# Kernel tuning notes

Measured on AMD Instinct MI355X. Metric: run time of the kernel, lower is better.

The kernel has to match this reference:

```python
import jax, jax.numpy as jnp
import numpy as np

B, K, G, C = 64, 4000, 200, 91
LAMBDA_BOX, LAMBDA_CLS, LAMBDA_OBJ = 5.0, 1.0, 1.0
EPS = 1e-9


def _make_boxes(key, lead_shape):
    k1, k2 = jax.random.split(key)
    tl = jax.random.uniform(k1, lead_shape + (2,)) * 0.7
    wh = jax.random.uniform(k2, lead_shape + (2,)) * 0.29 + 0.01
    return jnp.concatenate([tl, tl + wh], axis=-1)


def setup_inputs() -> dict:
    key = jax.random.key(0)
    ks = jax.random.split(key, 6)
    pred_boxes = _make_boxes(ks[0], (B, K))
    pred_obj_logits = jax.random.normal(ks[1], (B, K), dtype=jnp.float32)
    pred_cls_logits = jax.random.normal(ks[2], (B, K, C), dtype=jnp.float32)
    gt_boxes = _make_boxes(ks[3], (B, G))
    gt_labels = jax.random.randint(ks[4], (B, G), 0, C)
    n_gt = jax.random.randint(ks[5], (B,), 1, G + 1)
    gt_mask = jnp.arange(G)[None, :] < n_gt[:, None]
    return dict(pred_boxes=pred_boxes, pred_obj_logits=pred_obj_logits,
                pred_cls_logits=pred_cls_logits, gt_boxes=gt_boxes,
                gt_labels=gt_labels, gt_mask=gt_mask)


def _area(x):
    return jnp.clip(x[..., 2] - x[..., 0], 0.0) * jnp.clip(x[..., 3] - x[..., 1], 0.0)


def _pairwise_iou(a, b):
    # a: (K,4), b: (G,4) -> (K,G)
    tl = jnp.maximum(a[:, None, :2], b[None, :, :2])
    br = jnp.minimum(a[:, None, 2:], b[None, :, 2:])
    wh = jnp.clip(br - tl, 0.0)
    inter = wh[..., 0] * wh[..., 1]
    union = jnp.clip(_area(a)[:, None] + _area(b)[None, :] - inter, EPS)
    return inter / union


def _ciou_loss(pb, gb):
    # pb, gb: (M,4) matched pairs; elementwise CIoU loss = 1 - CIoU
    tl = jnp.maximum(pb[:, :2], gb[:, :2])
    br = jnp.minimum(pb[:, 2:], gb[:, 2:])
    wh = jnp.clip(br - tl, 0.0)
    inter = wh[:, 0] * wh[:, 1]
    iou = inter / jnp.clip(_area(pb) + _area(gb) - inter, EPS)
    px = (pb[:, 0] + pb[:, 2]) * 0.5
    py = (pb[:, 1] + pb[:, 3]) * 0.5
    tx = (gb[:, 0] + gb[:, 2]) * 0.5
    ty = (gb[:, 1] + gb[:, 3]) * 0.5
    rho2 = (px - tx) ** 2 + (py - ty) ** 2
    etl = jnp.minimum(pb[:, :2], gb[:, :2])
    ebr = jnp.maximum(pb[:, 2:], gb[:, 2:])
    c2 = jnp.clip((ebr[:, 0] - etl[:, 0]) ** 2 + (ebr[:, 1] - etl[:, 1]) ** 2, EPS)
    pw = jnp.clip(pb[:, 2] - pb[:, 0], EPS)
    ph = jnp.clip(pb[:, 3] - pb[:, 1], EPS)
    tw = jnp.clip(gb[:, 2] - gb[:, 0], EPS)
    th = jnp.clip(gb[:, 3] - gb[:, 1], EPS)
    v = (4.0 / jnp.pi ** 2) * (jnp.arctan(tw / th) - jnp.arctan(pw / ph)) ** 2
    alpha = jax.lax.stop_gradient(v / (1.0 - iou + v + EPS))  # torch.no_grad
    return 1.0 - (iou - rho2 / c2 - alpha * v)


def _greedy_match(iou0):
    # iou0: (K,G), invalid gt columns pre-masked to -1. Fixed min(K,G)-step
    # argmax-and-mask scan reproducing the torch greedy loop (break -> valid=False).
    Gd = iou0.shape[1]
    steps = min(iou0.shape[0], Gd)

    def step(m, _):
        flat = jnp.argmax(m)
        p = flat // Gd
        g = flat % Gd
        valid = m.reshape(-1)[flat] >= 0.0
        m2 = m.at[p, :].set(-1.0).at[:, g].set(-1.0)
        return jnp.where(valid, m2, m), (p, g, valid)

    _, (ps, gs, vs) = jax.lax.scan(step, iou0, None, length=steps)
    return ps, gs, vs


def _per_batch(pred_b, cls_b, gt_b, labels_b, mask_b):
    iou = jax.lax.stop_gradient(_pairwise_iou(pred_b, gt_b))  # matching is non-diff (.item() in torch)
    iou = jnp.where(mask_b[None, :], iou, -1.0)
    ps, gs, vs = _greedy_match(iou)
    vf = vs.astype(pred_b.dtype)
    n = jnp.sum(vf)
    denom = jnp.maximum(n, 1.0)
    pb = pred_b[ps]
    gb = gt_b[gs]
    lbox = jnp.sum(_ciou_loss(pb, gb) * vf) / denom
    logp = jax.nn.log_softmax(cls_b[ps], axis=-1)
    lce = -jnp.take_along_axis(logp, labels_b[gs][:, None], axis=1)[:, 0]
    lcls = jnp.sum(lce * vf) / denom
    obj_tgt = jnp.zeros((pred_b.shape[0],), pred_b.dtype).at[
        jnp.where(vs, ps, pred_b.shape[0])].set(1.0, mode='drop')
    return lbox, lcls, obj_tgt, n > 0.0


def reference(pred_boxes, pred_obj_logits, pred_cls_logits, gt_boxes, gt_labels, gt_mask):
    lbox_b, lcls_b, obj_tgt, has = jax.vmap(_per_batch)(
        pred_boxes, pred_cls_logits, gt_boxes, gt_labels, gt_mask)
    hf = has.astype(pred_boxes.dtype)
    nb = jnp.maximum(jnp.sum(hf), 1.0)
    loss_box = jnp.sum(lbox_b * hf) / nb
    loss_cls = jnp.sum(lcls_b * hf) / nb
    # BCEWithLogits(mean): softplus(x) - t*x
    loss_obj = jnp.mean(jax.nn.softplus(pred_obj_logits) - obj_tgt * pred_obj_logits)
    total = LAMBDA_BOX * loss_box + LAMBDA_CLS * loss_cls + LAMBDA_OBJ * loss_obj
    return total, loss_box, loss_cls, loss_obj
```

## Files before the change

### kernel.cpp

```cpp
#include <hip/hip_runtime.h>
#include <math.h>

#define B_ 64
#define K_ 4000
#define G_ 200
#define C_ 91
#define EPS_ 1e-9f
#define NW_ 16
#define DEPTH_ 32
typedef unsigned long long ull;

#define WS_FLAG 0
#define WS_PART 256
#define WS_TOP 327680

__device__ __forceinline__ float box_area(float4 a) {
#pragma clang fp contract(off)
  return fmaxf(a.z - a.x, 0.f) * fmaxf(a.w - a.y, 0.f);
}

__device__ __forceinline__ float iou_ab(float4 a, float aA, float4 b, float aB) {
#pragma clang fp contract(off)
  float tlx = fmaxf(a.x, b.x), tly = fmaxf(a.y, b.y);
  float brx = fminf(a.z, b.z), bry = fminf(a.w, b.w);
  float w = fmaxf(brx - tlx, 0.f), h = fmaxf(bry - tly, 0.f);
  float inter = w * h;
  float uni = fmaxf(aA + aB - inter, EPS_);
  return inter / uni;
}

__device__ __forceinline__ float ciou_loss(float4 p, float4 g) {
  float tlx = fmaxf(p.x, g.x), tly = fmaxf(p.y, g.y);
  float brx = fminf(p.z, g.z), bry = fminf(p.w, g.w);
  float w = fmaxf(brx - tlx, 0.f), h = fmaxf(bry - tly, 0.f);
  float inter = w * h;
  float areaP = fmaxf(p.z - p.x, 0.f) * fmaxf(p.w - p.y, 0.f);
  float areaG = fmaxf(g.z - g.x, 0.f) * fmaxf(g.w - g.y, 0.f);
  float iou = inter / fmaxf(areaP + areaG - inter, EPS_);
  float px = (p.x + p.z) * 0.5f, py = (p.y + p.w) * 0.5f;
  float tx = (g.x + g.z) * 0.5f, ty = (g.y + g.w) * 0.5f;
  float rho2 = (px - tx) * (px - tx) + (py - ty) * (py - ty);
  float ex = fmaxf(p.z, g.z) - fminf(p.x, g.x);
  float ey = fmaxf(p.w, g.w) - fminf(p.y, g.y);
  float c2 = fmaxf(ex * ex + ey * ey, EPS_);
  float pw = fmaxf(p.z - p.x, EPS_), ph = fmaxf(p.w - p.y, EPS_);
  float tw = fmaxf(g.z - g.x, EPS_), th = fmaxf(g.w - g.y, EPS_);
  float dat = atanf(tw / th) - atanf(pw / ph);
  float v = (4.0f / (float)(M_PI * M_PI)) * dat * dat;
  float alpha = v / ((1.f - iou) + v + EPS_);
  return 1.f - (iou - rho2 / c2 - alpha * v);
}

__global__ void kdetect(const unsigned char* m8, int* flag) {
  int b = threadIdx.x;
  int ok = 1;
  const unsigned char* r = m8 + b * G_;
  if (r[0] != 1) ok = 0;
  int seen0 = 0;
  for (int g = 0; g < G_; ++g) {
    unsigned char c = r[g];
    if (c > 1) { ok = 0; break; }
    if (c == 0) seen0 = 1;
    else if (seen0) { ok = 0; break; }
  }
  int all = __all(ok);
  if (b == 0) *flag = all ? 1 : 0;
}

__device__ __forceinline__ float block_sum(float v, float* s_red) {
  for (int off = 32; off > 0; off >>= 1) v += __shfl_xor(v, off);
  int lane = threadIdx.x & 63, wid = threadIdx.x >> 6;
  if (lane == 0) s_red[wid] = v;
  __syncthreads();
  float r = 0.f;
  if (wid == 0) {
    float t = (lane < NW_) ? s_red[lane] : 0.f;
    for (int off = 32; off > 0; off >>= 1) t += __shfl_xor(t, off);
    r = t;
  }
  __syncthreads();
  return r;
}

__device__ __forceinline__ ull wave_maxkey(ull k) {
  for (int off = 32; off > 0; off >>= 1) {
    ull o = __shfl_xor(k, off);
    if (o > k) k = o;
  }
  return k;
}

#define TOP4_INS(key)                                   \
  if ((key) > t3) {                                     \
    t3 = (key);                                         \
    ull tmp_;                                           \
    if (t3 > t2) { tmp_ = t2; t2 = t3; t3 = tmp_; }     \
    if (t2 > t1) { tmp_ = t1; t1 = t2; t2 = tmp_; }     \
    if (t1 > t0) { tmp_ = t0; t0 = t1; t1 = tmp_; }     \
  }

#define TOP8_INS(key)                                   \
  if ((key) > t7) {                                     \
    t7 = (key);                                         \
    ull tmp_;                                           \
    if (t7 > t6) { tmp_ = t6; t6 = t7; t7 = tmp_; }     \
    if (t6 > t5) { tmp_ = t5; t5 = t6; t6 = tmp_; }     \
    if (t5 > t4) { tmp_ = t4; t4 = t5; t5 = tmp_; }     \
    if (t4 > t3) { tmp_ = t3; t3 = t4; t4 = tmp_; }     \
    if (t3 > t2) { tmp_ = t2; t2 = t3; t3 = tmp_; }     \
    if (t2 > t1) { tmp_ = t1; t1 = t2; t2 = tmp_; }     \
    if (t1 > t0) { tmp_ = t0; t0 = t1; t1 = tmp_; }     \
  }

__global__ __launch_bounds__(1024) void kinit(const float* __restrict__ pred_boxes,
                                              const float* __restrict__ gt_boxes,
                                              const void* __restrict__ gt_mask,
                                              char* __restrict__ ws) {
  __shared__ float4 s_p[K_];
  const int blk = blockIdx.x;
  const int b = blk >> 3, oct = blk & 7;
  const int tid = threadIdx.x, lane = tid & 63, wid = tid >> 6;
  const int msk8 = *(const int*)(ws + WS_FLAG);
  const float4* p4 = (const float4*)pred_boxes + (size_t)b * K_;
  const float4* g4 = (const float4*)gt_boxes + (size_t)b * G_;

  for (int i = tid; i < K_; i += 1024) s_p[i] = p4[i];
  __syncthreads();

  ull* wtop = (ull*)(ws + WS_TOP);
  for (int cc = wid; cc < 25; cc += 16) {
    const int col = oct * 25 + cc;
    ull* dst = wtop + ((size_t)b * G_ + col) * DEPTH_;
    int v;
    if (msk8) v = ((const unsigned char*)gt_mask)[(size_t)b * G_ + col] != 0;
    else      v = ((const int*)gt_mask)[(size_t)b * G_ + col] != 0;
    if (!v) {
      for (int o = lane; o < DEPTH_; o += 64) dst[o] = 0ull;
      continue;
    }
    float4 gb = g4[col];
    float gA = box_area(gb);
    ull t0 = 0, t1 = 0, t2 = 0, t3 = 0;
#pragma unroll 2
    for (int k = lane; k < K_; k += 64) {
      float4 pb = s_p[k];
      float iou = iou_ab(pb, box_area(pb), gb, gA);
      ull e = ((ull)__float_as_uint(iou) << 12) | (ull)(4095 - k);
      TOP4_INS(e);
    }
    int supplied = 0, written = 0;
    for (int o = 0; o < DEPTH_; ++o) {
      ull m = wave_maxkey(t0);
      if (m == 0ull) break;
      int dn = 0;
      if (t0 == m) {
        t0 = t1; t1 = t2; t2 = t3; t3 = 0;
        if (++supplied == 4) dn = 1;
      }
      if (lane == 0) dst[o] = m;
      ++written;
      if (__any(dn)) break;
    }
    for (int o = written + lane; o < DEPTH_; o += 64) dst[o] = 0ull;
  }
}

__global__ __launch_bounds__(1024) void kmerged(
    const float* __restrict__ pred_boxes, const float* __restrict__ obj_logits,
    const float* __restrict__ cls_logits, const float* __restrict__ gt_boxes,
    const int* __restrict__ gt_labels, char* __restrict__ ws) {
  __shared__ float s_gx[G_], s_gy[G_], s_gz[G_], s_gw[G_], s_garea[G_];
  __shared__ unsigned char s_rowused[4096];
  __shared__ ull s_toplist[G_][DEPTH_ + 1];
  __shared__ int s_mp[G_];
  __shared__ unsigned short s_mg[G_];
  __shared__ int s_cnt;
  __shared__ float s_red[NW_];
  const int b = blockIdx.x;
  const int tid = threadIdx.x, lane = tid & 63, wid = tid >> 6;
  const float4* p4 = (const float4*)pred_boxes + (size_t)b * K_;
  const float4* g4 = (const float4*)gt_boxes + (size_t)b * G_;
  const ull* wtop = (const ull*)(ws + WS_TOP);

  for (int g = tid; g < G_; g += 1024) {
    float4 gb = g4[g];
    s_gx[g] = gb.x; s_gy[g] = gb.y; s_gz[g] = gb.z; s_gw[g] = gb.w;
    s_garea[g] = box_area(gb);
  }
  for (int k = tid; k < 4096; k += 1024) s_rowused[k] = 0;
  for (int i = tid; i < G_ * DEPTH_; i += 1024)
    s_toplist[i / DEPTH_][i % DEPTH_] = wtop[((size_t)b * G_) * DEPTH_ + i];
  __syncthreads();

  if (wid == 0) {
    ull key0 = 0, key1 = 0, key2 = 0, key3 = 0;
    int ptr0 = DEPTH_, ptr1 = DEPTH_, ptr2 = DEPTH_, ptr3 = DEPTH_;
    int cloc = 0;
#define SLOTINIT(S)                                                        \
    { int col = S * 64 + lane;                                             \
      if (col < G_) {                                                      \
        ull h_ = s_toplist[col][0];                                        \
        if (h_ != 0ull) {                                                  \
          key##S = (h_ << 8) | (ull)(255 - col); ptr##S = 1; ++cloc; } } }
    SLOTINIT(0) SLOTINIT(1) SLOTINIT(2) SLOTINIT(3)
#undef SLOTINIT
    for (int off = 32; off > 0; off >>= 1) cloc += __shfl_xor(cloc, off);
    const int cnt = cloc;
    if (lane == 0) s_cnt = cnt;

    for (int step = 0; step < cnt;) {
      ull a1 = key0, a2 = key1;
      if (key1 > key0) { a1 = key1; a2 = key0; }
      if (key2 > a1) { a2 = a1; a1 = key2; } else if (key2 > a2) a2 = key2;
      if (key3 > a1) { a2 = a1; a1 = key3; } else if (key3 > a2) a2 = key3;
      for (int off = 32; off > 0; off >>= 1) {
        ull b1 = __shfl_xor(a1, off), b2 = __shfl_xor(a2, off);
        if (b1 > a1) { a2 = (a1 > b2) ? a1 : b2; a1 = b1; }
        else { a2 = (b1 > a2) ? b1 : a2; }
      }
      const int p1 = 4095 - (int)((a1 >> 8) & 0xFFF);
      const int g1v = 255 - (int)(a1 & 0xFF);
      const int p2 = 4095 - (int)((a2 >> 8) & 0xFFF);
      const int g2v = 255 - (int)(a2 & 0xFF);
      const bool do2 = (a2 != 0ull) && (p2 != p1) && (step + 1 < cnt);
      if (lane == 0) {
        s_mp[step] = p1; s_mg[step] = (unsigned short)g1v; s_rowused[p1] = 1;
        if (do2) { s_mp[step + 1] = p2; s_mg[step + 1] = (unsigned short)g2v; s_rowused[p2] = 1; }
      }
      __builtin_amdgcn_wave_barrier();
      const int gd2 = do2 ? g2v : -1;
      const int pd2 = do2 ? p2 : -1;
      int need = 0;
#define DEMOTE(S)                                                           \
      { int col = S * 64 + lane; ull kk = key##S;                           \
        if (kk != 0ull) {                                                   \
          if (col == g1v || col == gd2) { key##S = 0ull; }                  \
          else { int krow = 4095 - (int)((kk >> 8) & 0xFFF);                \
            if (krow == p1 || krow == pd2) {                                \
              ull nk = 0ull; int np = ptr##S;                               \
              while (np < DEPTH_) {                                         \
                ull e = s_toplist[col][np]; ++np;                           \
                if (e == 0ull) { np = DEPTH_; break; }                      \
                int pr = 4095 - (int)((e >> 12) & 0xFFF);                   \
                if (!s_rowused[pr]) { nk = (e << 8) | (ull)(255 - col); break; } \
              }                                                             \
              ptr##S = np; key##S = nk;                                     \
              if (nk == 0ull) need |= (1 << S); } } } }
      DEMOTE(0) DEMOTE(1) DEMOTE(2) DEMOTE(3)
#undef DEMOTE
      while (__any(need)) {
        unsigned long long bal = __ballot(need != 0);
        int src = (int)__builtin_ctzll(bal);
        int myslot = need ? __builtin_ctz(need) : 0;
        int slot = __shfl(myslot, src);
        int col = slot * 64 + src;
        float4 gb = make_float4(s_gx[col], s_gy[col], s_gz[col], s_gw[col]);
        float gA = s_garea[col];
        ull t0 = 0, t1 = 0, t2 = 0, t3 = 0, t4 = 0, t5 = 0, t6 = 0, t7 = 0;
#pragma unroll 2
        for (int k = lane; k < K_; k += 64) {
          if (!s_rowused[k]) {
            float4 pb = p4[k];
            float iou = iou_ab(pb, box_area(pb), gb, gA);
            ull e = ((ull)__float_as_uint(iou) << 12) | (ull)(4095 - k);
            TOP8_INS(e);
          }
        }
        ull newhead = 0ull;
        int supplied = 0, written = 0;
        for (int o = 0; o < DEPTH_; ++o) {
          ull m = wave_maxkey(t0);
          if (m == 0ull) break;
          if (o == 0) newhead = m;
          int dn = 0;
          if (t0 == m) {
            t0 = t1; t1 = t2; t2 = t3; t3 = t4; t4 = t5; t5 = t6; t6 = t7; t7 = 0;
            if (++supplied == 8) dn = 1;
          }
          if (lane == src) s_toplist[col][o] = m;
          ++written;
          if (__any(dn)) break;
        }
        if (lane == src) {
          for (int o = written; o < DEPTH_; ++o) s_toplist[col][o] = 0ull;
          ull nk = newhead ? ((newhead << 8) | (ull)(255 - col)) : 0ull;
          if (slot == 0) { key0 = nk; ptr0 = 1; }
          else if (slot == 1) { key1 = nk; ptr1 = 1; }
          else if (slot == 2) { key2 = nk; ptr2 = 1; }
          else { key3 = nk; ptr3 = 1; }
          need &= ~(1 << slot);
        }
        __builtin_amdgcn_wave_barrier();
      }
      step += do2 ? 2 : 1;
    }
  }
  __syncthreads();

  const int cnt = s_cnt;
  float lbox = 0.f, lcls = 0.f;
  for (int i = tid; i < cnt; i += 1024) {
    int p = s_mp[i], g = s_mg[i];
    float4 pb = p4[p];
    float4 gb = make_float4(s_gx[g], s_gy[g], s_gz[g], s_gw[g]);
    lbox += ciou_loss(pb, gb);
    int label = gt_labels[(size_t)b * G_ + g];
    const float* lg = cls_logits + ((size_t)b * K_ + p) * C_;
    float m = -1e30f;
    for (int cc = 0; cc < C_; ++cc) m = fmaxf(m, lg[cc]);
    float s = 0.f;
    for (int cc = 0; cc < C_; ++cc) s += expf(lg[cc] - m);
    lcls += (m + logf(s)) - lg[label];
  }
  float obj = 0.f;
  const float* ol = obj_logits + (size_t)b * K_;
  for (int k = tid; k < K_; k += 1024) {
    float x = ol[k];
    float sp = fmaxf(x, 0.f) + log1pf(expf(-fabsf(x)));
    if (s_rowused[k]) sp -= x;
    obj += sp;
  }
  lbox = block_sum(lbox, s_red);
  lcls = block_sum(lcls, s_red);
  obj = block_sum(obj, s_red);
  if (tid == 0) {
    float* partials = (float*)(ws + WS_PART);
    float n = (float)cnt;
    float denom = fmaxf(n, 1.f);
    partials[b * 4 + 0] = lbox / denom;
    partials[b * 4 + 1] = lcls / denom;
    partials[b * 4 + 2] = obj;
    partials[b * 4 + 3] = (n > 0.f) ? 1.f : 0.f;
  }
}

__global__ void kfinal(const char* __restrict__ ws, float* __restrict__ out) {
  int b = threadIdx.x;
  const float* partials = (const float*)(ws + WS_PART);
  float lb = partials[b * 4 + 0], lc = partials[b * 4 + 1];
  float ob = partials[b * 4 + 2], hf = partials[b * 4 + 3];
  float sb = lb * hf, sc = lc * hf, sh = hf, so = ob;
  for (int off = 32; off > 0; off >>= 1) {
    sb += __shfl_xor(sb, off);
    sc += __shfl_xor(sc, off);
    sh += __shfl_xor(sh, off);
    so += __shfl_xor(so, off);
  }
  if (b == 0) {
    float nb = fmaxf(sh, 1.f);
    float box = sb / nb, cls = sc / nb;
    float obj = so / (float)(B_ * K_);
    out[0] = 5.f * box + cls + obj;
    out[1] = box;
    out[2] = cls;
    out[3] = obj;
  }
}

extern "C" void kernel_launch(void* const* d_in, const int* in_sizes, int n_in,
                              void* d_out, int out_size, void* d_ws, size_t ws_size,
                              hipStream_t stream) {
  const float* pred_boxes = (const float*)d_in[0];
  const float* obj_logits = (const float*)d_in[1];
  const float* cls_logits = (const float*)d_in[2];
  const float* gt_boxes = (const float*)d_in[3];
  const int* gt_labels = (const int*)d_in[4];
  const void* gt_mask = d_in[5];
  float* out = (float*)d_out;
  char* ws = (char*)d_ws;

  hipLaunchKernelGGL(kdetect, dim3(1), dim3(64), 0, stream,
                     (const unsigned char*)gt_mask, (int*)(ws + WS_FLAG));
  hipLaunchKernelGGL(kinit, dim3(B_ * 8), dim3(1024), 0, stream,
                     pred_boxes, gt_boxes, gt_mask, ws);
  hipLaunchKernelGGL(kmerged, dim3(B_), dim3(1024), 0, stream,
                     pred_boxes, obj_logits, cls_logits, gt_boxes, gt_labels, ws);
  hipLaunchKernelGGL(kfinal, dim3(1), dim3(64), 0, stream, ws, out);
}
```

Measured before the change: 259.3 us.

## Batch two GT columns per wave and rank-extract refill top-lists in parallel

```diff
diff --git a/kernel.cpp b/kernel.cpp
--- a/kernel.cpp
+++ b/kernel.cpp
@@ -90,7 +90,7 @@
   return k;
 }
 
-#define TOP4_INS(key)                                   \
+#define TOP4_INS(key, t0, t1, t2, t3)                   \
   if ((key) > t3) {                                     \
     t3 = (key);                                         \
     ull tmp_;                                           \
@@ -99,18 +99,23 @@
     if (t1 > t0) { tmp_ = t0; t0 = t1; t1 = tmp_; }     \
   }
 
-#define TOP8_INS(key)                                   \
-  if ((key) > t7) {                                     \
-    t7 = (key);                                         \
-    ull tmp_;                                           \
-    if (t7 > t6) { tmp_ = t6; t6 = t7; t7 = tmp_; }     \
-    if (t6 > t5) { tmp_ = t5; t5 = t6; t6 = tmp_; }     \
-    if (t5 > t4) { tmp_ = t4; t4 = t5; t5 = tmp_; }     \
-    if (t4 > t3) { tmp_ = t3; t3 = t4; t4 = tmp_; }     \
-    if (t3 > t2) { tmp_ = t2; t2 = t3; t3 = tmp_; }     \
-    if (t2 > t1) { tmp_ = t1; t1 = t2; t2 = tmp_; }     \
-    if (t1 > t0) { tmp_ = t0; t0 = t1; t1 = tmp_; }     \
-  }
+__device__ __forceinline__ void extract_list(ull t0, ull t1, ull t2, ull t3,
+                                             ull* dst, int lane) {
+  int supplied = 0, written = 0;
+  for (int o = 0; o < DEPTH_; ++o) {
+    ull m = wave_maxkey(t0);
+    if (m == 0ull) break;
+    int dn = 0;
+    if (t0 == m) {
+      t0 = t1; t1 = t2; t2 = t3; t3 = 0;
+      if (++supplied == 4) dn = 1;
+    }
+    if (lane == 0) dst[o] = m;
+    ++written;
+    if (__any(dn)) break;
+  }
+  for (int o = written + lane; o < DEPTH_; o += 64) dst[o] = 0ull;
+}
 
 __global__ __launch_bounds__(1024) void kinit(const float* __restrict__ pred_boxes,
                                               const float* __restrict__ gt_boxes,
@@ -127,41 +132,53 @@
   for (int i = tid; i < K_; i += 1024) s_p[i] = p4[i];
   __syncthreads();
 
+  const int base = oct * 25;
+  const int colA = base + wid;
+  const int colB = base + 16 + wid;
+  const bool hasB = (wid < 9);
   ull* wtop = (ull*)(ws + WS_TOP);
-  for (int cc = wid; cc < 25; cc += 16) {
-    const int col = oct * 25 + cc;
-    ull* dst = wtop + ((size_t)b * G_ + col) * DEPTH_;
-    int v;
-    if (msk8) v = ((const unsigned char*)gt_mask)[(size_t)b * G_ + col] != 0;
-    else      v = ((const int*)gt_mask)[(size_t)b * G_ + col] != 0;
-    if (!v) {
-      for (int o = lane; o < DEPTH_; o += 64) dst[o] = 0ull;
-      continue;
-    }
-    float4 gb = g4[col];
-    float gA = box_area(gb);
-    ull t0 = 0, t1 = 0, t2 = 0, t3 = 0;
+
+  int vA, vB = 0;
+  if (msk8) vA = ((const unsigned char*)gt_mask)[(size_t)b * G_ + colA] != 0;
+  else      vA = ((const int*)gt_mask)[(size_t)b * G_ + colA] != 0;
+  if (hasB) {
+    if (msk8) vB = ((const unsigned char*)gt_mask)[(size_t)b * G_ + colB] != 0;
+    else      vB = ((const int*)gt_mask)[(size_t)b * G_ + colB] != 0;
+  }
+
+  float4 gbA, gbB;
+  float gAA = 0.f, gAB = 0.f;
+  if (vA) { gbA = g4[colA]; gAA = box_area(gbA); }
+  if (vB) { gbB = g4[colB]; gAB = box_area(gbB); }
+
+  ull a0 = 0, a1 = 0, a2 = 0, a3 = 0;
+  ull b0 = 0, b1 = 0, b2 = 0, b3 = 0;
+  if (vA | vB) {
 #pragma unroll 2
     for (int k = lane; k < K_; k += 64) {
       float4 pb = s_p[k];
-      float iou = iou_ab(pb, box_area(pb), gb, gA);
-      ull e = ((ull)__float_as_uint(iou) << 12) | (ull)(4095 - k);
-      TOP4_INS(e);
+      float ar = box_area(pb);
+      if (vA) {
+        float iou = iou_ab(pb, ar, gbA, gAA);
+        ull e = ((ull)__float_as_uint(iou) << 12) | (ull)(4095 - k);
+        TOP4_INS(e, a0, a1, a2, a3);
+      }
+      if (vB) {
+        float iou = iou_ab(pb, ar, gbB, gAB);
+        ull e = ((ull)__float_as_uint(iou) << 12) | (ull)(4095 - k);
+        TOP4_INS(e, b0, b1, b2, b3);
+      }
     }
-    int supplied = 0, written = 0;
-    for (int o = 0; o < DEPTH_; ++o) {
-      ull m = wave_maxkey(t0);
-      if (m == 0ull) break;
-      int dn = 0;
-      if (t0 == m) {
-        t0 = t1; t1 = t2; t2 = t3; t3 = 0;
-        if (++supplied == 4) dn = 1;
-      }
-      if (lane == 0) dst[o] = m;
-      ++written;
-      if (__any(dn)) break;
-    }
-    for (int o = written + lane; o < DEPTH_; o += 64) dst[o] = 0ull;
+  }
+  {
+    ull* dstA = wtop + ((size_t)b * G_ + colA) * DEPTH_;
+    if (vA) extract_list(a0, a1, a2, a3, dstA, lane);
+    else    for (int o = lane; o < DEPTH_; o += 64) dstA[o] = 0ull;
+  }
+  if (hasB) {
+    ull* dstB = wtop + ((size_t)b * G_ + colB) * DEPTH_;
+    if (vB) extract_list(b0, b1, b2, b3, dstB, lane);
+    else    for (int o = lane; o < DEPTH_; o += 64) dstB[o] = 0ull;
   }
 }
 
@@ -256,34 +273,44 @@
         int col = slot * 64 + src;
         float4 gb = make_float4(s_gx[col], s_gy[col], s_gz[col], s_gw[col]);
         float gA = s_garea[col];
-        ull t0 = 0, t1 = 0, t2 = 0, t3 = 0, t4 = 0, t5 = 0, t6 = 0, t7 = 0;
+        ull t0 = 0, t1 = 0, t2 = 0, t3 = 0;
 #pragma unroll 2
         for (int k = lane; k < K_; k += 64) {
           if (!s_rowused[k]) {
             float4 pb = p4[k];
             float iou = iou_ab(pb, box_area(pb), gb, gA);
             ull e = ((ull)__float_as_uint(iou) << 12) | (ull)(4095 - k);
-            TOP8_INS(e);
+            TOP4_INS(e, t0, t1, t2, t3);
           }
         }
-        ull newhead = 0ull;
-        int supplied = 0, written = 0;
-        for (int o = 0; o < DEPTH_; ++o) {
-          ull m = wave_maxkey(t0);
-          if (m == 0ull) break;
-          if (o == 0) newhead = m;
-          int dn = 0;
-          if (t0 == m) {
-            t0 = t1; t1 = t2; t2 = t3; t3 = t4; t4 = t5; t5 = t6; t6 = t7; t7 = 0;
-            if (++supplied == 8) dn = 1;
-          }
-          if (lane == src) s_toplist[col][o] = m;
-          ++written;
-          if (__any(dn)) break;
+        int r0 = 0, r1 = 0, r2 = 0, r3 = 0;
+        for (int i = 0; i < 64; ++i) {
+          ull o0 = __shfl(t0, i), o1 = __shfl(t1, i);
+          ull o2 = __shfl(t2, i), o3 = __shfl(t3, i);
+          r0 += (o0 > t0) + (o1 > t0) + (o2 > t0) + (o3 > t0);
+          r1 += (o0 > t1) + (o1 > t1) + (o2 > t1) + (o3 > t1);
+          r2 += (o0 > t2) + (o1 > t2) + (o2 > t2) + (o3 > t2);
+          r3 += (o0 > t3) + (o1 > t3) + (o2 > t3) + (o3 > t3);
         }
+        int cut = (t3 != 0ull) ? (r3 + 1) : 0x7FFFFFFF;
+        int nc = (t0 != 0ull) + (t1 != 0ull) + (t2 != 0ull) + (t3 != 0ull);
+        for (int off = 32; off > 0; off >>= 1) {
+          int oc = __shfl_xor(cut, off);
+          cut = (oc < cut) ? oc : cut;
+          nc += __shfl_xor(nc, off);
+        }
+        const int Lf = (cut < DEPTH_) ? cut : DEPTH_;
+        const int zstart = (Lf < nc) ? Lf : nc;
+        if (t0 != 0ull && r0 < Lf) s_toplist[col][r0] = t0;
+        if (t1 != 0ull && r1 < Lf) s_toplist[col][r1] = t1;
+        if (t2 != 0ull && r2 < Lf) s_toplist[col][r2] = t2;
+        if (t3 != 0ull && r3 < Lf) s_toplist[col][r3] = t3;
+        for (int o = lane; o < DEPTH_; o += 64)
+          if (o >= zstart) s_toplist[col][o] = 0ull;
+        __builtin_amdgcn_wave_barrier();
+        ull newhead = s_toplist[col][0];
         if (lane == src) {
-          for (int o = written; o < DEPTH_; ++o) s_toplist[col][o] = 0ull;
-          ull nk = newhead ? ((newhead << 8) | (ull)(255 - col)) : 0ull;
+          ull nk = (newhead << 8) | (ull)(255 - col);
           if (slot == 0) { key0 = nk; ptr0 = 1; }
           else if (slot == 1) { key1 = nk; ptr1 = 1; }
           else if (slot == 2) { key2 = nk; ptr2 = 1; }
```

New measurement: 256.0 us. About the same (-1.3%).
